# Performance work log

Measured on AMD Instinct MI355X. Metric: run time of the kernel, lower is better.

Reference implementation:

```python
import jax, jax.numpy as jnp
import numpy as np

B, C, H, W = 8, 4, 384, 384


def setup_inputs() -> dict:
    key = jax.random.key(0)
    k1, k2 = jax.random.split(key)
    outputs = jax.random.normal(k1, (B, C, H, W), dtype=jnp.float32)
    targets = jax.random.randint(k2, (B, H, W), 0, C)  # every class present w.h.p.
    return {"outputs": outputs, "targets": targets}


def _edt(is_zero):
    """Exact 2D Euclidean distance transform, batched.

    is_zero: bool [B,C,H,W], True at 'feature' pixels (distance 0 there).
    Returns float32 [B,C,H,W] distance to nearest True pixel.
    Separable exact algorithm (Meijster/Felzenszwalb-Huttenlocher style):
      phase 1: 1D distance along H via forward+backward scans;
      phase 2: dt^2(x,y) = min_j g(x,j)^2 + (y-j)^2 via a scan over y.
    """
    b, c, h, w = is_zero.shape
    BIG = jnp.float32(h + w)  # finite sentinel (exceeds any true distance)

    def pass1(carry, z):
        d = jnp.where(z, jnp.float32(0.0), jnp.minimum(carry + 1.0, BIG))
        return d, d

    init = jnp.full((b, c, w), BIG, jnp.float32)
    zt = jnp.moveaxis(is_zero, 2, 0)  # [H,B,C,W]
    _, fwd = jax.lax.scan(pass1, init, zt)
    _, bwd = jax.lax.scan(pass1, init, zt[::-1])
    g = jnp.minimum(fwd, bwd[::-1])          # [H,B,C,W] vertical 1D distances
    g2 = jnp.moveaxis(g * g, 0, 2)           # [B,C,H,W]

    j = jnp.arange(w, dtype=jnp.float32)     # candidate columns

    def pass2(_, y):
        # min over j of g(x,j)^2 + (y-j)^2  -> [B,C,H]
        return 0, jnp.min(g2 + (y - j) ** 2, axis=-1)

    _, dt2 = jax.lax.scan(pass2, 0, j)       # [W,B,C,H]
    return jnp.sqrt(jnp.moveaxis(dt2, 0, 3))  # [B,C,H,W]


def reference(outputs, targets):
    num_classes = outputs.shape[1]
    # one-hot: true_hot[b,c,h,w] = (targets[b,h,w] == c)
    true_hot = targets[:, None, :, :] == jnp.arange(num_classes)[None, :, None, None]
    dt = _edt(true_hot)                                  # 0 at class pixels
    dmax = jnp.max(dt, axis=(2, 3), keepdims=True)       # per (b,c) slice max
    dist_map = jnp.where(true_hot, -dmax, dt)            # factor = -1
    # weight=None -> ones(C); weight_matrix/weight.sum() == 1/C
    loss = jax.nn.softmax(outputs, axis=1) * dist_map / jnp.float32(num_classes)
    return jnp.mean(loss)
```

## Files before the change

### kernel.cpp

```cpp
#include <hip/hip_runtime.h>

#define B 8
#define C 4
#define H 384
#define W 384
#define HW (H * W)
#define CHW (C * H * W)
#define NTOT (B * CHW)
#define BIG2 589824
#define TPI 144
#define NBLK (B * TPI)
#define NSEG (B * H * 6)
#define LOG2E 1.44269504088896340736f

__device__ __forceinline__ int nearest2(unsigned long long m, int lx, int shl) {
    unsigned long long right = m >> lx;
    int dR = right ? (int)__builtin_ctzll(right) : 999;
    unsigned long long leftb = m << shl;
    int dL = leftb ? (int)__builtin_clzll(leftb) : 999;
    int d = min(dR, dL);
    return d * d;
}

__device__ __forceinline__ int scan32f(unsigned int right, unsigned int left, int add) {
    int dR = __builtin_ctz(right | 0x80000000u);
    int dL = __builtin_clz(left | 1u);
    int d = min(dR, dL);
    return d * d + add;
}

__device__ __attribute__((noinline))
int ring_fallback(const int* __restrict__ tg, int xa, int ya, int c, int best) {
    for (int d = 17; d * d < best; ++d) {
        int xlo = xa - d, xhi = xa + d, ylo = ya - d, yhi = ya + d;
        for (int xx = max(xlo, 0); xx <= min(xhi, W - 1); ++xx) {
            int ddx = xx - xa;
            int bb = ddx * ddx + d * d;
            if (bb < best) {
                if (ylo >= 0 && tg[ylo * W + xx] == c) best = bb;
                if (yhi < H && tg[yhi * W + xx] == c) best = min(best, bb);
            }
        }
        for (int yy = max(ylo + 1, 0); yy <= min(yhi - 1, H - 1); ++yy) {
            int ddy = yy - ya;
            int bb = ddy * ddy + d * d;
            if (bb < best) {
                if (xlo >= 0 && tg[yy * W + xlo] == c) best = bb;
                if (xhi < W && tg[yy * W + xhi] == c) best = min(best, bb);
            }
        }
    }
    return best;
}

__global__ __launch_bounds__(256)
void build_masks(const int* __restrict__ targets,
                 unsigned long long* __restrict__ masks) {
    int wv = threadIdx.x >> 6, lane = threadIdx.x & 63;
    int seg = blockIdx.x * 4 + wv;
    if (seg >= NSEG) return;
    int wd = seg % 6, rem = seg / 6;
    int tv = targets[rem * W + wd * 64 + lane];
    unsigned long long m0 = __ballot(tv == 0);
    unsigned long long m1 = __ballot(tv == 1);
    unsigned long long m2 = __ballot(tv == 2);
    unsigned long long m3 = __ballot(tv == 3);
    if (lane == 0) {
        unsigned long long* dst = masks + (size_t)rem * 24 + wd;
        dst[0]  = m0;
        dst[6]  = m1;
        dst[12] = m2;
        dst[18] = m3;
    }
}

__global__ __launch_bounds__(512)
void dist_loss_kernel(const float* __restrict__ outputs,
                      const int* __restrict__ targets,
                      const unsigned long long* __restrict__ masks,
                      float* __restrict__ parts) {
    __shared__ unsigned long long rowsm[64][4];
    __shared__ unsigned long long big[32 * 18];
    __shared__ float sred[8][9];

    int bid = blockIdx.x;
    int bx = bid % 12, by = (bid / 12) % 12, b = bid / TPI;
    int x0 = bx * 32, y0 = by * 32;
    int tid = threadIdx.x, lane = tid & 63, wv = tid >> 6;
    const int* tg = targets + b * HW;

    int x2 = (tid & 15) * 2;
    int y = tid >> 4;
    int ya = y0 + y, ly = y + 16;

    const float* ob = outputs + (size_t)b * CHW + (size_t)ya * W + (x0 + x2);
    float2 f0 = *(const float2*)ob;
    float2 f1 = *(const float2*)(ob + HW);
    float2 f2 = *(const float2*)(ob + 2 * HW);
    float2 f3 = *(const float2*)(ob + 3 * HW);

    if (tid < 256) {
        int r = tid >> 2, cc = tid & 3;
        int yaS = y0 - 16 + r;
        unsigned long long wmask = 0ull;
        if (yaS >= 0 && yaS < H) {
            const unsigned long long* mrow =
                masks + ((size_t)(b * H + yaS)) * 24 + cc * 6;
            int bitpos = x0 - 16;
            int iw = bitpos >> 6, sh = bitpos & 63;
            unsigned long long lo = (iw >= 0) ? mrow[iw] : 0ull;
            unsigned long long hi = (iw + 1 < 6) ? mrow[iw + 1] : 0ull;
            wmask = (lo >> sh) | (hi << (64 - sh));
        }
        rowsm[r][cc] = wmask;
    }
    __syncthreads();

    {
        int yy = tid >> 4, c = (tid >> 2) & 3, lvl = tid & 3;
        unsigned long long v = (lvl == 0)
            ? rowsm[16 + yy][c]
            : (rowsm[16 + yy - lvl][c] | rowsm[16 + yy + lvl][c]);
        big[yy * 18 + c * 4 + lvl] = v;
    }
    __syncthreads();

    float red[9];
    #pragma unroll
    for (int j = 0; j < 9; ++j) red[j] = 0.0f;

    float pr[4][2];
    {
        const float* fc0 = (const float*)&f0;
        const float* fc1 = (const float*)&f1;
        const float* fc2 = (const float*)&f2;
        const float* fc3 = (const float*)&f3;
        #pragma unroll
        for (int p = 0; p < 2; ++p) {
            float e0 = exp2f(fc0[p] * LOG2E);
            float e1 = exp2f(fc1[p] * LOG2E);
            float e2 = exp2f(fc2[p] * LOG2E);
            float e3 = exp2f(fc3[p] * LOG2E);
            float inv = 1.0f / (e0 + e1 + e2 + e3);
            pr[0][p] = e0 * inv; pr[1][p] = e1 * inv;
            pr[2][p] = e2 * inv; pr[3][p] = e3 * inv;
        }
    }

    #pragma unroll
    for (int c = 0; c < 4; ++c) {
        const ulonglong2* pp = (const ulonglong2*)&big[y * 18 + c * 4];
        ulonglong2 va = pp[0], vb = pp[1];
        unsigned long long r0 = va.x >> x2;
        unsigned long long r1 = va.y >> x2;
        unsigned long long r2 = vb.x >> x2;
        unsigned long long r3 = vb.y >> x2;
        unsigned int l0 = (unsigned int)r0, l1 = (unsigned int)r1;
        unsigned int l2 = (unsigned int)r2, l3 = (unsigned int)r3;
        #pragma unroll
        for (int p = 0; p < 2; ++p) {
            unsigned int w0r = (unsigned int)(r0 >> (16 + p));
            unsigned int w1r = (unsigned int)(r1 >> (16 + p));
            unsigned int w2r = (unsigned int)(r2 >> (16 + p));
            unsigned int w3r = (unsigned int)(r3 >> (16 + p));
            unsigned int w0l = l0 << (15 - p);
            unsigned int w1l = l1 << (15 - p);
            unsigned int w2l = l2 << (15 - p);
            unsigned int w3l = l3 << (15 - p);
            int best = scan32f(w0r, w0l, 0);
            best = min(best, scan32f(w1r, w1l, 1));
            best = min(best, scan32f(w2r, w2l, 4));
            best = min(best, scan32f(w3r, w3l, 9));
            if (best > 16) {
                int lx = 16 + x2 + p, shl = 63 - lx;
                for (int dy = 4; dy <= 16 && dy * dy < best; ++dy) {
                    unsigned long long mm = rowsm[ly + dy][c] | rowsm[ly - dy][c];
                    if (mm) best = min(best, dy * dy + nearest2(mm, lx, shl));
                }
                if (best > 289) {
                    if (best >= 961) best = BIG2;
                    best = ring_fallback(tg, x0 + x2 + p, ya, c, best);
                }
            }
            float dt = sqrtf((float)best);
            red[0] += pr[c][p] * dt;
            if (w0r & 1u) red[1 + c] += pr[c][p];
            red[5 + c] = fmaxf(red[5 + c], dt);
        }
    }

    #pragma unroll
    for (int off = 32; off > 0; off >>= 1) {
        #pragma unroll
        for (int j = 0; j < 5; ++j) red[j] += __shfl_down(red[j], off);
        #pragma unroll
        for (int j = 5; j < 9; ++j) red[j] = fmaxf(red[j], __shfl_down(red[j], off));
    }
    if (lane == 0) {
        #pragma unroll
        for (int j = 0; j < 9; ++j) sred[wv][j] = red[j];
    }
    __syncthreads();

    if (wv == 0) {
        float v[9];
        #pragma unroll
        for (int j = 0; j < 9; ++j) v[j] = (lane < 8) ? sred[lane][j] : 0.0f;
        #pragma unroll
        for (int off = 4; off > 0; off >>= 1) {
            #pragma unroll
            for (int j = 0; j < 5; ++j) v[j] += __shfl_down(v[j], off);
            #pragma unroll
            for (int j = 5; j < 9; ++j) v[j] = fmaxf(v[j], __shfl_down(v[j], off));
        }
        if (lane == 0) {
            #pragma unroll
            for (int j = 0; j < 9; ++j) parts[j * NBLK + bid] = v[j];
        }
    }
}

__global__ __launch_bounds__(256)
void finalize(const float* __restrict__ parts, float* __restrict__ out) {
    __shared__ double asum[4];
    __shared__ double Tsh[32];
    __shared__ float Msh[32];
    int tid = threadIdx.x, lane = tid & 63, wv = tid >> 6;

    double a = 0.0;
    for (int i = tid; i < NBLK; i += 256) a += (double)parts[i];
    #pragma unroll
    for (int off = 32; off > 0; off >>= 1) a += __shfl_down(a, off);
    if (lane == 0) asum[wv] = a;

    for (int k = 0; k < 8; ++k) {
        int s = wv * 8 + k;
        int bb = s >> 2, cc = s & 3;
        double ts = 0.0;
        float ms = 0.0f;
        for (int i = lane; i < TPI; i += 64) {
            int blk = bb * TPI + i;
            ts += (double)parts[(1 + cc) * NBLK + blk];
            ms = fmaxf(ms, parts[(5 + cc) * NBLK + blk]);
        }
        #pragma unroll
        for (int off = 32; off > 0; off >>= 1) {
            ts += __shfl_down(ts, off);
            ms = fmaxf(ms, __shfl_down(ms, off));
        }
        if (lane == 0) { Tsh[s] = ts; Msh[s] = ms; }
    }
    __syncthreads();
    if (tid == 0) {
        double A = asum[0] + asum[1] + asum[2] + asum[3];
        double st = 0.0;
        for (int s = 0; s < 32; ++s) st += (double)Msh[s] * Tsh[s];
        out[0] = (float)((A - st) / ((double)C * (double)NTOT));
    }
}

extern "C" void kernel_launch(void* const* d_in, const int* in_sizes, int n_in,
                              void* d_out, int out_size, void* d_ws, size_t ws_size,
                              hipStream_t stream) {
    const float* outputs = (const float*)d_in[0];
    const int* targets = (const int*)d_in[1];
    float* out = (float*)d_out;
    float* parts = (float*)d_ws;
    unsigned long long* masks =
        (unsigned long long*)((char*)d_ws + 64 * 1024);

    build_masks<<<NSEG / 4, 256, 0, stream>>>(targets, masks);
    dist_loss_kernel<<<NBLK, 512, 0, stream>>>(outputs, targets, masks, parts);
    finalize<<<1, 256, 0, stream>>>(parts, out);
}
```

Baseline: 93.18 us.

## Fuse class bitmask construction into main kernel via per-block ballots

Drops the separate build_masks kernel and its global mask buffer. Each block now reads its 64x64 target halo window directly and builds the per-class row bitmasks in shared memory with wavefront ballots, using a clamped, validity-masked path for edge tiles. This removes a kernel launch and a global write/read round trip, at the cost of redundant target reads across overlapping block halos.

Result: slower. 96.63 us (+3.7%).

```diff
diff --git a/kernel.cpp b/kernel.cpp
--- a/kernel.cpp
+++ b/kernel.cpp
@@ -10,7 +10,6 @@
 #define BIG2 589824
 #define TPI 144
 #define NBLK (B * TPI)
-#define NSEG (B * H * 6)
 #define LOG2E 1.44269504088896340736f
 
 __device__ __forceinline__ int nearest2(unsigned long long m, int lx, int shl) {
@@ -53,31 +52,9 @@
     return best;
 }
 
-__global__ __launch_bounds__(256)
-void build_masks(const int* __restrict__ targets,
-                 unsigned long long* __restrict__ masks) {
-    int wv = threadIdx.x >> 6, lane = threadIdx.x & 63;
-    int seg = blockIdx.x * 4 + wv;
-    if (seg >= NSEG) return;
-    int wd = seg % 6, rem = seg / 6;
-    int tv = targets[rem * W + wd * 64 + lane];
-    unsigned long long m0 = __ballot(tv == 0);
-    unsigned long long m1 = __ballot(tv == 1);
-    unsigned long long m2 = __ballot(tv == 2);
-    unsigned long long m3 = __ballot(tv == 3);
-    if (lane == 0) {
-        unsigned long long* dst = masks + (size_t)rem * 24 + wd;
-        dst[0]  = m0;
-        dst[6]  = m1;
-        dst[12] = m2;
-        dst[18] = m3;
-    }
-}
-
 __global__ __launch_bounds__(512)
 void dist_loss_kernel(const float* __restrict__ outputs,
                       const int* __restrict__ targets,
-                      const unsigned long long* __restrict__ masks,
                       float* __restrict__ parts) {
     __shared__ unsigned long long rowsm[64][4];
     __shared__ unsigned long long big[32 * 18];
@@ -99,20 +76,38 @@
     float2 f2 = *(const float2*)(ob + 2 * HW);
     float2 f3 = *(const float2*)(ob + 3 * HW);
 
-    if (tid < 256) {
-        int r = tid >> 2, cc = tid & 3;
-        int yaS = y0 - 16 + r;
-        unsigned long long wmask = 0ull;
-        if (yaS >= 0 && yaS < H) {
-            const unsigned long long* mrow =
-                masks + ((size_t)(b * H + yaS)) * 24 + cc * 6;
-            int bitpos = x0 - 16;
-            int iw = bitpos >> 6, sh = bitpos & 63;
-            unsigned long long lo = (iw >= 0) ? mrow[iw] : 0ull;
-            unsigned long long hi = (iw + 1 < 6) ? mrow[iw + 1] : 0ull;
-            wmask = (lo >> sh) | (hi << (64 - sh));
-        }
-        rowsm[r][cc] = wmask;
+    bool edge = (bx == 0) | (bx == 11) | (by == 0) | (by == 11);
+    if (!edge) {
+        const int* tp = tg + (y0 - 16 + wv) * W + (x0 - 16 + lane);
+        #pragma unroll
+        for (int i = 0; i < 8; ++i) {
+            int r = i * 8 + wv;
+            int tv = tp[i * 8 * W];
+            unsigned long long m0 = __ballot(tv == 0);
+            unsigned long long m1 = __ballot(tv == 1);
+            unsigned long long m2 = __ballot(tv == 2);
+            unsigned long long m3 = __ballot(tv == 3);
+            if (lane == 0) {
+                rowsm[r][0] = m0; rowsm[r][1] = m1;
+                rowsm[r][2] = m2; rowsm[r][3] = m3;
+            }
+        }
+    } else {
+        for (int i = 0; i < 8; ++i) {
+            int r = i * 8 + wv;
+            int yr = y0 - 16 + r, xr = x0 - 16 + lane;
+            bool valid = (yr >= 0) & (yr < H) & (xr >= 0) & (xr < W);
+            int yc = min(max(yr, 0), H - 1), xc = min(max(xr, 0), W - 1);
+            int tv = tg[yc * W + xc];
+            unsigned long long m0 = __ballot(valid && tv == 0);
+            unsigned long long m1 = __ballot(valid && tv == 1);
+            unsigned long long m2 = __ballot(valid && tv == 2);
+            unsigned long long m3 = __ballot(valid && tv == 3);
+            if (lane == 0) {
+                rowsm[r][0] = m0; rowsm[r][1] = m1;
+                rowsm[r][2] = m2; rowsm[r][3] = m3;
+            }
+        }
     }
     __syncthreads();
 
@@ -266,10 +261,7 @@
     const int* targets = (const int*)d_in[1];
     float* out = (float*)d_out;
     float* parts = (float*)d_ws;
-    unsigned long long* masks =
-        (unsigned long long*)((char*)d_ws + 64 * 1024);
-
-    build_masks<<<NSEG / 4, 256, 0, stream>>>(targets, masks);
-    dist_loss_kernel<<<NBLK, 512, 0, stream>>>(outputs, targets, masks, parts);
+
+    dist_loss_kernel<<<NBLK, 512, 0, stream>>>(outputs, targets, parts);
     finalize<<<1, 256, 0, stream>>>(parts, out);
 }
```
